# Kernel tuning notes

Measured on AMD Instinct MI355X. Metric: run time of the kernel, lower is better.

## Reference

```python
import jax, jax.numpy as jnp
import numpy as np

NUM_HEADS = 4
NUM_GROUPS = 8
EPS = 1e-5


def group_norm(x, gamma, beta):
    # x: [b, c, h, w], GroupNorm with NUM_GROUPS groups, eps=1e-5
    b, c, h, w = x.shape
    xg = x.reshape(b, NUM_GROUPS, (c // NUM_GROUPS) * h * w)
    mean = jnp.mean(xg, axis=-1, keepdims=True)
    var = jnp.var(xg, axis=-1, keepdims=True)
    xn = ((xg - mean) * jax.lax.rsqrt(var + EPS)).reshape(b, c, h, w)
    return xn * gamma[None, :, None, None] + beta[None, :, None, None]


def setup_inputs() -> dict:
    key = jax.random.key(0)
    ks = jax.random.split(key, 4)
    b, c, h, w = 4, 256, 64, 64
    x = jax.random.normal(ks[0], (b, c, h, w), dtype=jnp.float32)
    gamma = jnp.ones((c,), dtype=jnp.float32)
    beta = jnp.zeros((c,), dtype=jnp.float32)
    w_qkv = jax.random.normal(ks[1], (3 * c, c), dtype=jnp.float32) * (c ** -0.5)
    b_qkv = jnp.zeros((3 * c,), dtype=jnp.float32)
    w_proj = jax.random.normal(ks[2], (c, c), dtype=jnp.float32) * (c ** -0.5)
    b_proj = jnp.zeros((c,), dtype=jnp.float32)
    return {"x": x, "gamma": gamma, "beta": beta, "w_qkv": w_qkv,
            "b_qkv": b_qkv, "w_proj": w_proj, "b_proj": b_proj}


def reference(x, gamma, beta, w_qkv, b_qkv, w_proj, b_proj):
    b, c, h, w = x.shape
    heads = NUM_HEADS
    dim = c // heads
    n = h * w
    residual = x
    xn = group_norm(x, gamma, beta)
    # 1x1 conv == per-pixel linear: [b,c,h,w] x [3c,c] -> [b,3c,h,w]
    qkv = jnp.einsum('bchw,oc->bohw', xn, w_qkv) + b_qkv[None, :, None, None]
    # channel layout: (three, heads, dim)
    qkv = qkv.reshape(b, 3, heads, dim, n)            # [b,3,H,D,N]
    qkv = jnp.transpose(qkv, (1, 0, 2, 4, 3))         # [3,b,H,N,D]
    q, k, v = qkv[0], qkv[1], qkv[2]
    scale = dim ** -0.5
    scores = jnp.einsum('bhid,bhjd->bhij', q * scale, k)  # [b,H,N,N]
    attn = jax.nn.softmax(scores, axis=-1)
    out = jnp.einsum('bhij,bhjd->bhid', attn, v)          # [b,H,N,D]
    out = jnp.transpose(out, (0, 1, 3, 2)).reshape(b, c, h, w)
    out = jnp.einsum('bchw,oc->bohw', out, w_proj) + b_proj[None, :, None, None]
    return out + residual
```

## Files before the change

kernel.cpp:

```cpp
#include <hip/hip_runtime.h>
#include <stdint.h>

typedef unsigned short ushort_t;
typedef __attribute__((ext_vector_type(8))) short bf16x8;
typedef __attribute__((ext_vector_type(4))) float f32x4;

__device__ __forceinline__ ushort_t f2bf(float f) {
  union { float f; unsigned u; } v; v.f = f;
  unsigned r = v.u + 0x7fffu + ((v.u >> 16) & 1u);
  return (ushort_t)(r >> 16);
}
__device__ __forceinline__ unsigned bfbits(float f) {
  union { float f; unsigned u; } v; v.f = f; return v.u;
}
__device__ __forceinline__ unsigned pack_trunc(float lo, float hi) {
#if __has_builtin(__builtin_amdgcn_perm)
  return __builtin_amdgcn_perm(bfbits(hi), bfbits(lo), 0x07060302u);
#else
  return (bfbits(lo) >> 16) | (bfbits(hi) & 0xffff0000u);
#endif
}
__device__ __forceinline__ unsigned pack_rn(float lo, float hi) {
  return (unsigned)f2bf(lo) | ((unsigned)f2bf(hi) << 16);
}

#define SCALE_Q 0.18033688011112042f
#define EXP_BIAS 23.083109273961734f

__global__ __launch_bounds__(256)
void gn_stats1(const float* __restrict__ x, float2* __restrict__ partial) {
  int blk = blockIdx.x, tid = threadIdx.x;
  const float* base = x + (size_t)blk * 16384;
  float s = 0.f, ss = 0.f;
  for (int i = tid * 4; i < 16384; i += 1024) {
    float4 v = *(const float4*)(base + i);
    s  += v.x + v.y + v.z + v.w;
    ss += v.x*v.x + v.y*v.y + v.z*v.z + v.w*v.w;
  }
  __shared__ float rs[256], rss[256];
  rs[tid] = s; rss[tid] = ss;
  __syncthreads();
  for (int off = 128; off > 0; off >>= 1) {
    if (tid < off) { rs[tid] += rs[tid+off]; rss[tid] += rss[tid+off]; }
    __syncthreads();
  }
  if (tid == 0) partial[blk] = make_float2(rs[0], rss[0]);
}

__global__ __launch_bounds__(64)
void gn_stats2(const float2* __restrict__ partial, float* __restrict__ stats) {
  int g = threadIdx.x;
  if (g < 32) {
    float s = 0.f, ss = 0.f;
    #pragma unroll
    for (int k = 0; k < 8; k++) { float2 p = partial[g*8 + k]; s += p.x; ss += p.y; }
    float mean = s * (1.f/131072.f);
    float var  = ss * (1.f/131072.f) - mean*mean;
    stats[g*2]   = mean;
    stats[g*2+1] = rsqrtf(var + 1e-5f);
  }
}

__global__ __launch_bounds__(256)
void gn_apply_t(const float* __restrict__ x, const float* __restrict__ stats,
                const float* __restrict__ gamma, const float* __restrict__ beta,
                ushort_t* __restrict__ xn_t, int b0) {
  int blk = blockIdx.x;
  int tid = threadIdx.x;
  int ct = blk & 7;
  int nt = (blk >> 3) & 15;
  int bl = blk >> 7;
  int b  = b0 + bl;
  int c0 = ct * 32;
  float mean = stats[(b*8 + ct)*2];
  float rstd = stats[(b*8 + ct)*2 + 1];
  __shared__ ushort_t Ls[32][264];
  for (int idx = tid; idx < 32*64; idx += 256) {
    int cc = idx >> 6, seg = idx & 63;
    float ga = gamma[c0+cc], be = beta[c0+cc];
    float a = rstd * ga;
    float bb = be - mean * a;
    float4 v = *(const float4*)(x + ((size_t)(b*256 + c0 + cc))*4096 + nt*256 + seg*4);
    ushort4 t4 = make_ushort4(f2bf(v.x*a+bb), f2bf(v.y*a+bb), f2bf(v.z*a+bb), f2bf(v.w*a+bb));
    *(ushort4*)&Ls[cc][seg*4] = t4;
  }
  __syncthreads();
  for (int idx = tid; idx < 256*4; idx += 256) {
    int n = idx >> 2, seg = idx & 3;
    union { ushort_t u[8]; uint4 v; } pk;
    #pragma unroll
    for (int e = 0; e < 8; e++) pk.u[e] = Ls[seg*8 + e][n];
    *(uint4*)(xn_t + ((size_t)(bl*4096 + nt*256 + n))*256 + c0 + seg*8) = pk.v;
  }
}

__global__ __launch_bounds__(256)
void wconv2(const float* __restrict__ wq, const float* __restrict__ wp,
            ushort_t* __restrict__ oq, ushort_t* __restrict__ op) {
  int blk = blockIdx.x;
  const float* w; ushort_t* o; int i;
  if (blk < 192) { w = wq; o = oq; i = blk*256 + threadIdx.x; }
  else           { w = wp; o = op; i = (blk-192)*256 + threadIdx.x; }
  float4 v = *(const float4*)(w + (size_t)i*4);
  *(ushort4*)(o + (size_t)i*4) = make_ushort4(f2bf(v.x), f2bf(v.y), f2bf(v.z), f2bf(v.w));
}

__global__ __launch_bounds__(256)
void gemm_qkv(const ushort_t* __restrict__ A, const ushort_t* __restrict__ Bt,
              const float* __restrict__ bias, ushort_t* __restrict__ q,
              ushort_t* __restrict__ kbuf, ushort_t* __restrict__ vt, int b0) {
  int blk = blockIdx.x;
  int nt = blk % 12, mt = blk / 12;
  int m0 = mt*128, n0 = nt*64;
  int tid = threadIdx.x;
  int wave = tid >> 6, lane = tid & 63, quad = lane >> 4, l16 = lane & 15;
  __shared__ ushort_t As[128][40];
  __shared__ ushort_t Bs[64][40];
  __shared__ ushort_t Lt[64][136];
  f32x4 acc[2][4];
  #pragma unroll
  for (int i = 0; i < 2; i++)
    #pragma unroll
    for (int j = 0; j < 4; j++) acc[i][j] = (f32x4){0.f,0.f,0.f,0.f};

  for (int k0 = 0; k0 < 256; k0 += 32) {
    #pragma unroll
    for (int i = tid; i < 512; i += 256) {
      int row = i >> 2, seg = i & 3;
      *(uint4*)&As[row][seg*8] = *(const uint4*)(A + (size_t)(m0+row)*256 + k0 + seg*8);
    }
    {
      int row = tid >> 2, seg = tid & 3;
      *(uint4*)&Bs[row][seg*8] = *(const uint4*)(Bt + (size_t)(n0+row)*256 + k0 + seg*8);
    }
    __syncthreads();
    bf16x8 af[2], bfr[4];
    #pragma unroll
    for (int t = 0; t < 2; t++) af[t]  = *(const bf16x8*)&As[wave*32 + t*16 + l16][quad*8];
    #pragma unroll
    for (int t = 0; t < 4; t++) bfr[t] = *(const bf16x8*)&Bs[t*16 + l16][quad*8];
    #pragma unroll
    for (int ti = 0; ti < 2; ti++)
      #pragma unroll
      for (int jn = 0; jn < 4; jn++)
        acc[ti][jn] = __builtin_amdgcn_mfma_f32_16x16x32_bf16(af[ti], bfr[jn], acc[ti][jn], 0, 0, 0);
    __syncthreads();
  }

  int region = nt >> 2;
  if (region == 0) {
    #pragma unroll
    for (int jn = 0; jn < 4; jn++) {
      int n = n0 + jn*16 + l16;
      float bv = bias[n];
      #pragma unroll
      for (int ti = 0; ti < 2; ti++) {
        int mrow = m0 + wave*32 + ti*16 + quad*4;
        #pragma unroll
        for (int r = 0; r < 4; r++)
          q[(size_t)(b0*4096 + mrow + r)*256 + n] = f2bf((acc[ti][jn][r] + bv) * SCALE_Q);
      }
    }
  } else if (region == 1) {
    #pragma unroll
    for (int jn = 0; jn < 4; jn++) {
      int n = n0 + jn*16 + l16;
      float bv = bias[n];
      #pragma unroll
      for (int ti = 0; ti < 2; ti++) {
        int mrow = m0 + wave*32 + ti*16 + quad*4;
        #pragma unroll
        for (int r = 0; r < 4; r++)
          kbuf[(size_t)(b0*4096 + mrow + r)*256 + (n - 256)] = f2bf(acc[ti][jn][r] + bv);
      }
    }
  } else {
    int hh = nt - 8;
    int b_loc = m0 >> 12;
    #pragma unroll
    for (int jn = 0; jn < 4; jn++) {
      int n = n0 + jn*16 + l16;
      float bv = bias[n];
      int drow = jn*16 + l16;
      #pragma unroll
      for (int ti = 0; ti < 2; ti++) {
        int tcol = wave*32 + ti*16 + quad*4;
        uint2 w;
        w.x = pack_rn(acc[ti][jn][0] + bv, acc[ti][jn][1] + bv);
        w.y = pack_rn(acc[ti][jn][2] + bv, acc[ti][jn][3] + bv);
        *(uint2*)&Lt[drow][tcol] = w;
      }
    }
    __syncthreads();
    size_t vb_ = ((size_t)((b0 + b_loc)*4 + hh)*64)*4096 + (size_t)(m0 & 4095);
    for (int idx = tid; idx < 1024; idx += 256) {
      int dd = idx >> 4, toff = (idx & 15)*8;
      *(uint4*)(vt + vb_ + (size_t)dd*4096 + toff) = *(const uint4*)&Lt[dd][toff];
    }
  }
}

__global__ __launch_bounds__(256, 2)
void attn(ushort_t* __restrict__ q, const ushort_t* __restrict__ k,
          const ushort_t* __restrict__ vt) {
  int blk = blockIdx.x;
  int it = blk & 31;
  int h  = (blk >> 5) & 3;
  int b  = blk >> 7;
  int i0 = it * 128;
  int tid = threadIdx.x;
  int wave = tid >> 6, lane = tid & 63, quad = lane >> 4, l16 = lane & 15;

  __shared__ ushort_t Ks[2][128][68];
  __shared__ ushort_t Vs[2][64][132];
  __shared__ ushort_t Ps[4][16][72];

  ushort_t* qbase = q + (size_t)(b*4096 + i0)*256 + h*64;
  const ushort_t* kbase = k + (size_t)(b*4096)*256 + h*64;
  const ushort_t* vbase = vt + (size_t)(b*4 + h)*64*4096;

  bf16x8 qa[2][2];
  #pragma unroll
  for (int t = 0; t < 2; t++)
    #pragma unroll
    for (int kk = 0; kk < 2; kk++) {
      uint4 u = *(const uint4*)(qbase + (size_t)(wave*32 + t*16 + l16)*256 + kk*32 + quad*8);
      qa[t][kk] = *(const bf16x8*)&u;
    }

  bf16x8 ones;
  #pragma unroll
  for (int e = 0; e < 8; e++) ones[e] = (short)0x3F80;

  f32x4 o_acc[2][4];
  f32x4 l_acc[2];
  #pragma unroll
  for (int t = 0; t < 2; t++) {
    l_acc[t] = (f32x4){0.f,0.f,0.f,0.f};
    #pragma unroll
    for (int d = 0; d < 4; d++) o_acc[t][d] = (f32x4){0.f,0.f,0.f,0.f};
  }

  int sj = tid >> 3, sseg = (tid & 7)*8;
  uint4 rk[4], rv[4];
  #define LOADK(JT) { int j0n = (JT)*128; \
    rk[0] = *(const uint4*)(kbase + (size_t)(j0n + sj      )*256 + sseg); \
    rk[1] = *(const uint4*)(kbase + (size_t)(j0n + sj + 32 )*256 + sseg); \
    rk[2] = *(const uint4*)(kbase + (size_t)(j0n + sj + 64 )*256 + sseg); \
    rk[3] = *(const uint4*)(kbase + (size_t)(j0n + sj + 96 )*256 + sseg); }
  #define LOADV(JT) { int j0n = (JT)*128; \
    rv[0] = *(const uint4*)(vbase + (size_t)(sj     )*4096 + j0n + sseg); \
    rv[1] = *(const uint4*)(vbase + (size_t)(sj     )*4096 + j0n + 64 + sseg); \
    rv[2] = *(const uint4*)(vbase + (size_t)(sj + 32)*4096 + j0n + sseg); \
    rv[3] = *(const uint4*)(vbase + (size_t)(sj + 32)*4096 + j0n + 64 + sseg); }
  #define WRITEK(BI) { \
    *(uint4*)&Ks[BI][sj      ][sseg] = rk[0]; \
    *(uint4*)&Ks[BI][sj + 32 ][sseg] = rk[1]; \
    *(uint4*)&Ks[BI][sj + 64 ][sseg] = rk[2]; \
    *(uint4*)&Ks[BI][sj + 96 ][sseg] = rk[3]; }
  #define WRITEV(BI) { \
    *(uint4*)&Vs[BI][sj     ][sseg] = rv[0]; \
    *(uint4*)&Vs[BI][sj     ][64 + sseg] = rv[1]; \
    *(uint4*)&Vs[BI][sj + 32][sseg] = rv[2]; \
    *(uint4*)&Vs[BI][sj + 32][64 + sseg] = rv[3]; }

  #define COMPUTE_SUB(BI, jb) { \
    bf16x8 kb[4][2], vb[4][2]; \
    _Pragma("unroll") \
    for (int jn = 0; jn < 4; jn++) \
      _Pragma("unroll") \
      for (int kk = 0; kk < 2; kk++) { \
        kb[jn][kk] = *(const bf16x8*)&Ks[BI][(jb) + jn*16 + l16][kk*32 + quad*8]; \
        vb[jn][kk] = *(const bf16x8*)&Vs[BI][jn*16 + l16][(jb) + kk*32 + quad*8]; \
      } \
    _Pragma("unroll") \
    for (int t = 0; t < 2; t++) { \
      f32x4 s[4]; \
      _Pragma("unroll") \
      for (int jn = 0; jn < 4; jn++) { \
        f32x4 a4 = (f32x4){-EXP_BIAS, -EXP_BIAS, -EXP_BIAS, -EXP_BIAS}; \
        _Pragma("unroll") \
        for (int kk = 0; kk < 2; kk++) \
          a4 = __builtin_amdgcn_mfma_f32_16x16x32_bf16(kb[jn][kk], qa[t][kk], a4, 0, 0, 0); \
        s[jn] = a4; \
      } \
      _Pragma("unroll") \
      for (int jn = 0; jn < 4; jn++) { \
        float p0 = __builtin_exp2f(s[jn][0]); \
        float p1 = __builtin_exp2f(s[jn][1]); \
        float p2 = __builtin_exp2f(s[jn][2]); \
        float p3 = __builtin_exp2f(s[jn][3]); \
        uint2 w; \
        w.x = pack_trunc(p0, p1); \
        w.y = pack_trunc(p2, p3); \
        *(uint2*)&Ps[wave][l16][jn*16 + quad*4] = w; \
      } \
      bf16x8 pa[2]; \
      _Pragma("unroll") \
      for (int kk = 0; kk < 2; kk++) \
        pa[kk] = *(const bf16x8*)&Ps[wave][l16][kk*32 + quad*8]; \
      _Pragma("unroll") \
      for (int dn = 0; dn < 4; dn++) \
        _Pragma("unroll") \
        for (int kk = 0; kk < 2; kk++) \
          o_acc[t][dn] = __builtin_amdgcn_mfma_f32_16x16x32_bf16(vb[dn][kk], pa[kk], o_acc[t][dn], 0, 0, 0); \
      _Pragma("unroll") \
      for (int kk = 0; kk < 2; kk++) \
        l_acc[t] = __builtin_amdgcn_mfma_f32_16x16x32_bf16(ones, pa[kk], l_acc[t], 0, 0, 0); \
    } }

  LOADK(0); LOADV(0); WRITEK(0); WRITEV(0);
  __syncthreads();

  for (int jt = 0; jt < 32; jt++) {
    int cur = jt & 1;
    if (jt < 31) LOADK(jt + 1);
    COMPUTE_SUB(cur, 0);
    if (jt < 31) { WRITEK(cur ^ 1); LOADV(jt + 1); }
    COMPUTE_SUB(cur, 64);
    if (jt < 31) WRITEV(cur ^ 1);
    __syncthreads();
  }
  #undef LOADK
  #undef LOADV
  #undef WRITEK
  #undef WRITEV
  #undef COMPUTE_SUB

  #pragma unroll
  for (int t = 0; t < 2; t++) {
    float inv = 1.f / l_acc[t][0];
    size_t row = (size_t)(b*4096 + i0 + wave*32 + t*16 + l16)*256 + h*64;
    #pragma unroll
    for (int dn = 0; dn < 4; dn++) {
      ushort4 u;
      u.x = f2bf(o_acc[t][dn][0]*inv); u.y = f2bf(o_acc[t][dn][1]*inv);
      u.z = f2bf(o_acc[t][dn][2]*inv); u.w = f2bf(o_acc[t][dn][3]*inv);
      *(ushort4*)(q + row + dn*16 + quad*4) = u;
    }
  }
}

__global__ __launch_bounds__(256)
void gemm_proj(const ushort_t* __restrict__ A,
               const ushort_t* __restrict__ Bt,
               const float* __restrict__ bias, const float* __restrict__ resid,
               float* __restrict__ out, int col_base) {
  int blk = blockIdx.x;
  int mt = blk & 1, nt = blk >> 1;
  int m0 = mt*128, n0 = nt*64;
  int tid = threadIdx.x;
  int wave = tid >> 6, lane = tid & 63, quad = lane >> 4, l16 = lane & 15;
  __shared__ ushort_t As[128][40];
  __shared__ ushort_t Bs[64][40];
  f32x4 acc[2][4];
  #pragma unroll
  for (int i = 0; i < 2; i++)
    #pragma unroll
    for (int j = 0; j < 4; j++) acc[i][j] = (f32x4){0.f,0.f,0.f,0.f};

  for (int k0 = 0; k0 < 256; k0 += 32) {
    #pragma unroll
    for (int i = tid; i < 512; i += 256) {
      int row = i >> 2, seg = i & 3;
      *(uint4*)&As[row][seg*8] = *(const uint4*)(A + (size_t)(m0+row)*256 + k0 + seg*8);
    }
    {
      int row = tid >> 2, seg = tid & 3;
      *(uint4*)&Bs[row][seg*8] = *(const uint4*)(Bt + (size_t)(n0+row)*256 + k0 + seg*8);
    }
    __syncthreads();
    bf16x8 af[2], bfr[4];
    #pragma unroll
    for (int t = 0; t < 2; t++) af[t]  = *(const bf16x8*)&As[wave*32 + t*16 + l16][quad*8];
    #pragma unroll
    for (int t = 0; t < 4; t++) bfr[t] = *(const bf16x8*)&Bs[t*16 + l16][quad*8];
    #pragma unroll
    for (int ti = 0; ti < 2; ti++)
      #pragma unroll
      for (int jn = 0; jn < 4; jn++)
        acc[ti][jn] = __builtin_amdgcn_mfma_f32_16x16x32_bf16(af[ti], bfr[jn], acc[ti][jn], 0, 0, 0);
    __syncthreads();
  }
  #pragma unroll
  for (int jn = 0; jn < 4; jn++) {
    int col = col_base + n0 + jn*16 + l16;
    int bb = col >> 12;
    int np = col & 4095;
    #pragma unroll
    for (int ti = 0; ti < 2; ti++) {
      int o = m0 + wave*32 + ti*16 + quad*4;
      #pragma unroll
      for (int r = 0; r < 4; r++) {
        int oo = o + r;
        size_t addr = ((size_t)(bb*256 + oo))*4096 + np;
        out[addr] = acc[ti][jn][r] + bias[oo] + resid[addr];
      }
    }
  }
}

extern "C" void kernel_launch(void* const* d_in, const int* in_sizes, int n_in,
                              void* d_out, int out_size, void* d_ws, size_t ws_size,
                              hipStream_t stream) {
  const float* x      = (const float*)d_in[0];
  const float* gamma  = (const float*)d_in[1];
  const float* beta   = (const float*)d_in[2];
  const float* w_qkv  = (const float*)d_in[3];
  const float* b_qkv  = (const float*)d_in[4];
  const float* w_proj = (const float*)d_in[5];
  const float* b_proj = (const float*)d_in[6];
  float* out = (float*)d_out;

  char* ws = (char*)d_ws;
  float*  stats    = (float*)ws;
  float2* partial  = (float2*)(ws + 1024);
  ushort_t* wqkv_bf  = (ushort_t*)(ws + 4096);
  ushort_t* wproj_bf = (ushort_t*)(ws + 397312);
  char* big = ws + 528384;

  gn_stats1<<<dim3(256), dim3(256), 0, stream>>>(x, partial);
  gn_stats2<<<dim3(1), dim3(64), 0, stream>>>(partial, stats);
  wconv2<<<dim3(256), dim3(256), 0, stream>>>(w_qkv, w_proj, wqkv_bf, wproj_bf);

  if (ws_size >= (size_t)528384 + 3*(size_t)8388608 + (size_t)4194304) {
    ushort_t* q    = (ushort_t*)big;
    ushort_t* kbuf = (ushort_t*)(big + (size_t)8388608);
    ushort_t* vt   = (ushort_t*)(big + (size_t)16777216);
    ushort_t* xn   = (ushort_t*)(big + (size_t)25165824);
    for (int c = 0; c < 2; c++) {
      int b0 = c * 2;
      gn_apply_t<<<dim3(256), dim3(256), 0, stream>>>(x, stats, gamma, beta, xn, b0);
      gemm_qkv<<<dim3(768), dim3(256), 0, stream>>>(xn, wqkv_bf, b_qkv, q, kbuf, vt, b0);
    }
    attn<<<dim3(512), dim3(256), 0, stream>>>(q, kbuf, vt);
    gemm_proj<<<dim3(512), dim3(256), 0, stream>>>(wproj_bf, q, b_proj, x, out, 0);
  } else {
    ushort_t* q_c  = (ushort_t*)big;
    ushort_t* k_c  = (ushort_t*)(big + (size_t)2097152);
    ushort_t* vt_c = (ushort_t*)(big + (size_t)4194304);
    ushort_t* xn_c = (ushort_t*)(big + (size_t)6291456);
    for (int b0 = 0; b0 < 4; b0++) {
      gn_apply_t<<<dim3(128), dim3(256), 0, stream>>>(x, stats, gamma, beta, xn_c, b0);
      gemm_qkv<<<dim3(384), dim3(256), 0, stream>>>(xn_c, wqkv_bf, b_qkv, q_c, k_c, vt_c, 0);
      attn<<<dim3(128), dim3(256), 0, stream>>>(q_c, k_c, vt_c);
      gemm_proj<<<dim3(128), dim3(256), 0, stream>>>(wproj_bf, q_c, b_proj, x, out, b0*4096);
    }
  }
}
```

Before: 256.4 us.

## Rewrite attention inner loop with 32x32x16 MFMA and register-resident P

```diff
diff --git a/kernel.cpp b/kernel.cpp
--- a/kernel.cpp
+++ b/kernel.cpp
@@ -4,6 +4,7 @@
 typedef unsigned short ushort_t;
 typedef __attribute__((ext_vector_type(8))) short bf16x8;
 typedef __attribute__((ext_vector_type(4))) float f32x4;
+typedef __attribute__((ext_vector_type(16))) float f32x16;
 
 __device__ __forceinline__ ushort_t f2bf(float f) {
   union { float f; unsigned u; } v; v.f = f;
@@ -22,6 +23,14 @@
 }
 __device__ __forceinline__ unsigned pack_rn(float lo, float hi) {
   return (unsigned)f2bf(lo) | ((unsigned)f2bf(hi) << 16);
+}
+__device__ __forceinline__ void swap32(unsigned &a, unsigned &b) {
+#if __has_builtin(__builtin_amdgcn_permlane32_swap)
+  auto r = __builtin_amdgcn_permlane32_swap(a, b, false, false);
+  a = r[0]; b = r[1];
+#else
+  asm volatile("v_permlane32_swap_b32 %0, %1" : "+v"(a), "+v"(b));
+#endif
 }
 
 #define SCALE_Q 0.18033688011112042f
@@ -209,105 +218,94 @@
   int b  = blk >> 7;
   int i0 = it * 128;
   int tid = threadIdx.x;
-  int wave = tid >> 6, lane = tid & 63, quad = lane >> 4, l16 = lane & 15;
-
-  __shared__ ushort_t Ks[2][128][68];
-  __shared__ ushort_t Vs[2][64][132];
-  __shared__ ushort_t Ps[4][16][72];
-
-  ushort_t* qbase = q + (size_t)(b*4096 + i0)*256 + h*64;
+  int wave = tid >> 6, lane = tid & 63;
+  int q32 = lane & 31, hi = lane >> 5;
+
+  __shared__ ushort_t Ks[2][128][72];
+  __shared__ ushort_t Vs[2][64][144];
+
   const ushort_t* kbase = k + (size_t)(b*4096)*256 + h*64;
   const ushort_t* vbase = vt + (size_t)(b*4 + h)*64*4096;
-
-  bf16x8 qa[2][2];
-  #pragma unroll
-  for (int t = 0; t < 2; t++)
-    #pragma unroll
-    for (int kk = 0; kk < 2; kk++) {
-      uint4 u = *(const uint4*)(qbase + (size_t)(wave*32 + t*16 + l16)*256 + kk*32 + quad*8);
-      qa[t][kk] = *(const bf16x8*)&u;
-    }
-
-  bf16x8 ones;
-  #pragma unroll
-  for (int e = 0; e < 8; e++) ones[e] = (short)0x3F80;
-
-  f32x4 o_acc[2][4];
-  f32x4 l_acc[2];
-  #pragma unroll
-  for (int t = 0; t < 2; t++) {
-    l_acc[t] = (f32x4){0.f,0.f,0.f,0.f};
-    #pragma unroll
-    for (int d = 0; d < 4; d++) o_acc[t][d] = (f32x4){0.f,0.f,0.f,0.f};
-  }
-
-  int sj = tid >> 3, sseg = (tid & 7)*8;
+  ushort_t* qrow = q + (size_t)(b*4096 + i0 + wave*32 + q32)*256 + h*64;
+
+  bf16x8 qb[4];
+  #pragma unroll
+  for (int s = 0; s < 4; s++) {
+    uint4 u = *(const uint4*)(qrow + s*16 + hi*8);
+    qb[s] = *(const bf16x8*)&u;
+  }
+
+  f32x16 o_acc[2];
+  #pragma unroll
+  for (int d = 0; d < 2; d++)
+    #pragma unroll
+    for (int r = 0; r < 16; r++) o_acc[d][r] = 0.f;
+  float lsum = 0.f;
+
+  int sr = tid >> 3, sc = (tid & 7) * 8;
+  int vr = tid >> 4, vc = (tid & 15) * 8;
   uint4 rk[4], rv[4];
   #define LOADK(JT) { int j0n = (JT)*128; \
-    rk[0] = *(const uint4*)(kbase + (size_t)(j0n + sj      )*256 + sseg); \
-    rk[1] = *(const uint4*)(kbase + (size_t)(j0n + sj + 32 )*256 + sseg); \
-    rk[2] = *(const uint4*)(kbase + (size_t)(j0n + sj + 64 )*256 + sseg); \
-    rk[3] = *(const uint4*)(kbase + (size_t)(j0n + sj + 96 )*256 + sseg); }
+    rk[0] = *(const uint4*)(kbase + (size_t)(j0n + sr      )*256 + sc); \
+    rk[1] = *(const uint4*)(kbase + (size_t)(j0n + sr + 32 )*256 + sc); \
+    rk[2] = *(const uint4*)(kbase + (size_t)(j0n + sr + 64 )*256 + sc); \
+    rk[3] = *(const uint4*)(kbase + (size_t)(j0n + sr + 96 )*256 + sc); }
+  #define WRITEK(BI) { \
+    *(uint4*)&Ks[BI][sr      ][sc] = rk[0]; \
+    *(uint4*)&Ks[BI][sr + 32 ][sc] = rk[1]; \
+    *(uint4*)&Ks[BI][sr + 64 ][sc] = rk[2]; \
+    *(uint4*)&Ks[BI][sr + 96 ][sc] = rk[3]; }
   #define LOADV(JT) { int j0n = (JT)*128; \
-    rv[0] = *(const uint4*)(vbase + (size_t)(sj     )*4096 + j0n + sseg); \
-    rv[1] = *(const uint4*)(vbase + (size_t)(sj     )*4096 + j0n + 64 + sseg); \
-    rv[2] = *(const uint4*)(vbase + (size_t)(sj + 32)*4096 + j0n + sseg); \
-    rv[3] = *(const uint4*)(vbase + (size_t)(sj + 32)*4096 + j0n + 64 + sseg); }
-  #define WRITEK(BI) { \
-    *(uint4*)&Ks[BI][sj      ][sseg] = rk[0]; \
-    *(uint4*)&Ks[BI][sj + 32 ][sseg] = rk[1]; \
-    *(uint4*)&Ks[BI][sj + 64 ][sseg] = rk[2]; \
-    *(uint4*)&Ks[BI][sj + 96 ][sseg] = rk[3]; }
+    rv[0] = *(const uint4*)(vbase + (size_t)(vr     )*4096 + j0n + vc); \
+    rv[1] = *(const uint4*)(vbase + (size_t)(vr + 16)*4096 + j0n + vc); \
+    rv[2] = *(const uint4*)(vbase + (size_t)(vr + 32)*4096 + j0n + vc); \
+    rv[3] = *(const uint4*)(vbase + (size_t)(vr + 48)*4096 + j0n + vc); }
   #define WRITEV(BI) { \
-    *(uint4*)&Vs[BI][sj     ][sseg] = rv[0]; \
-    *(uint4*)&Vs[BI][sj     ][64 + sseg] = rv[1]; \
-    *(uint4*)&Vs[BI][sj + 32][sseg] = rv[2]; \
-    *(uint4*)&Vs[BI][sj + 32][64 + sseg] = rv[3]; }
-
-  #define COMPUTE_SUB(BI, jb) { \
-    bf16x8 kb[4][2], vb[4][2]; \
+    *(uint4*)&Vs[BI][vr     ][vc] = rv[0]; \
+    *(uint4*)&Vs[BI][vr + 16][vc] = rv[1]; \
+    *(uint4*)&Vs[BI][vr + 32][vc] = rv[2]; \
+    *(uint4*)&Vs[BI][vr + 48][vc] = rv[3]; }
+
+  #define COMPUTE_SUB32(BI, JB) { \
+    bf16x8 kb0 = *(const bf16x8*)&Ks[BI][(JB) + q32][hi*8]; \
+    bf16x8 kb1 = *(const bf16x8*)&Ks[BI][(JB) + q32][16 + hi*8]; \
+    bf16x8 kb2 = *(const bf16x8*)&Ks[BI][(JB) + q32][32 + hi*8]; \
+    bf16x8 kb3 = *(const bf16x8*)&Ks[BI][(JB) + q32][48 + hi*8]; \
+    f32x16 s_; \
     _Pragma("unroll") \
-    for (int jn = 0; jn < 4; jn++) \
-      _Pragma("unroll") \
-      for (int kk = 0; kk < 2; kk++) { \
-        kb[jn][kk] = *(const bf16x8*)&Ks[BI][(jb) + jn*16 + l16][kk*32 + quad*8]; \
-        vb[jn][kk] = *(const bf16x8*)&Vs[BI][jn*16 + l16][(jb) + kk*32 + quad*8]; \
-      } \
+    for (int r = 0; r < 16; r++) s_[r] = -EXP_BIAS; \
+    s_ = __builtin_amdgcn_mfma_f32_32x32x16_bf16(kb0, qb[0], s_, 0, 0, 0); \
+    s_ = __builtin_amdgcn_mfma_f32_32x32x16_bf16(kb1, qb[1], s_, 0, 0, 0); \
+    s_ = __builtin_amdgcn_mfma_f32_32x32x16_bf16(kb2, qb[2], s_, 0, 0, 0); \
+    s_ = __builtin_amdgcn_mfma_f32_32x32x16_bf16(kb3, qb[3], s_, 0, 0, 0); \
+    float pt[16]; \
     _Pragma("unroll") \
-    for (int t = 0; t < 2; t++) { \
-      f32x4 s[4]; \
-      _Pragma("unroll") \
-      for (int jn = 0; jn < 4; jn++) { \
-        f32x4 a4 = (f32x4){-EXP_BIAS, -EXP_BIAS, -EXP_BIAS, -EXP_BIAS}; \
-        _Pragma("unroll") \
-        for (int kk = 0; kk < 2; kk++) \
-          a4 = __builtin_amdgcn_mfma_f32_16x16x32_bf16(kb[jn][kk], qa[t][kk], a4, 0, 0, 0); \
-        s[jn] = a4; \
-      } \
-      _Pragma("unroll") \
-      for (int jn = 0; jn < 4; jn++) { \
-        float p0 = __builtin_exp2f(s[jn][0]); \
-        float p1 = __builtin_exp2f(s[jn][1]); \
-        float p2 = __builtin_exp2f(s[jn][2]); \
-        float p3 = __builtin_exp2f(s[jn][3]); \
-        uint2 w; \
-        w.x = pack_trunc(p0, p1); \
-        w.y = pack_trunc(p2, p3); \
-        *(uint2*)&Ps[wave][l16][jn*16 + quad*4] = w; \
-      } \
-      bf16x8 pa[2]; \
-      _Pragma("unroll") \
-      for (int kk = 0; kk < 2; kk++) \
-        pa[kk] = *(const bf16x8*)&Ps[wave][l16][kk*32 + quad*8]; \
-      _Pragma("unroll") \
-      for (int dn = 0; dn < 4; dn++) \
-        _Pragma("unroll") \
-        for (int kk = 0; kk < 2; kk++) \
-          o_acc[t][dn] = __builtin_amdgcn_mfma_f32_16x16x32_bf16(vb[dn][kk], pa[kk], o_acc[t][dn], 0, 0, 0); \
-      _Pragma("unroll") \
-      for (int kk = 0; kk < 2; kk++) \
-        l_acc[t] = __builtin_amdgcn_mfma_f32_16x16x32_bf16(ones, pa[kk], l_acc[t], 0, 0, 0); \
-    } }
+    for (int r = 0; r < 16; r++) { \
+      float pe = __builtin_exp2f(s_[r]); \
+      s_[r] = pe; \
+      union { unsigned u; float f; } tv; tv.u = bfbits(pe) & 0xffff0000u; \
+      pt[r] = tv.f; \
+    } \
+    lsum += ((((pt[0]+pt[1])+(pt[2]+pt[3])) + ((pt[4]+pt[5])+(pt[6]+pt[7]))) \
+          + (((pt[8]+pt[9])+(pt[10]+pt[11])) + ((pt[12]+pt[13])+(pt[14]+pt[15])))); \
+    unsigned pkA = pack_trunc(s_[0],  s_[1]),  pkB = pack_trunc(s_[2],  s_[3]); \
+    unsigned pkC = pack_trunc(s_[4],  s_[5]),  pkD = pack_trunc(s_[6],  s_[7]); \
+    unsigned pkE = pack_trunc(s_[8],  s_[9]),  pkF = pack_trunc(s_[10], s_[11]); \
+    unsigned pkG = pack_trunc(s_[12], s_[13]), pkH = pack_trunc(s_[14], s_[15]); \
+    swap32(pkA, pkC); swap32(pkB, pkD);    \
+    swap32(pkE, pkG); swap32(pkF, pkH);    \
+    union { unsigned u[4]; bf16x8 v; } pb0_, pb1_; \
+    pb0_.u[0] = pkA; pb0_.u[1] = pkB; pb0_.u[2] = pkC; pb0_.u[3] = pkD; \
+    pb1_.u[0] = pkE; pb1_.u[1] = pkF; pb1_.u[2] = pkG; pb1_.u[3] = pkH; \
+    bf16x8 vb00 = *(const bf16x8*)&Vs[BI][q32     ][(JB) + hi*8]; \
+    bf16x8 vb01 = *(const bf16x8*)&Vs[BI][q32     ][(JB) + 16 + hi*8]; \
+    bf16x8 vb10 = *(const bf16x8*)&Vs[BI][32 + q32][(JB) + hi*8]; \
+    bf16x8 vb11 = *(const bf16x8*)&Vs[BI][32 + q32][(JB) + 16 + hi*8]; \
+    o_acc[0] = __builtin_amdgcn_mfma_f32_32x32x16_bf16(vb00, pb0_.v, o_acc[0], 0, 0, 0); \
+    o_acc[0] = __builtin_amdgcn_mfma_f32_32x32x16_bf16(vb01, pb1_.v, o_acc[0], 0, 0, 0); \
+    o_acc[1] = __builtin_amdgcn_mfma_f32_32x32x16_bf16(vb10, pb0_.v, o_acc[1], 0, 0, 0); \
+    o_acc[1] = __builtin_amdgcn_mfma_f32_32x32x16_bf16(vb11, pb1_.v, o_acc[1], 0, 0, 0); \
+  }
 
   LOADK(0); LOADV(0); WRITEK(0); WRITEV(0);
   __syncthreads();
@@ -315,9 +313,11 @@
   for (int jt = 0; jt < 32; jt++) {
     int cur = jt & 1;
     if (jt < 31) LOADK(jt + 1);
-    COMPUTE_SUB(cur, 0);
+    COMPUTE_SUB32(cur, 0)
+    COMPUTE_SUB32(cur, 32)
     if (jt < 31) { WRITEK(cur ^ 1); LOADV(jt + 1); }
-    COMPUTE_SUB(cur, 64);
+    COMPUTE_SUB32(cur, 64)
+    COMPUTE_SUB32(cur, 96)
     if (jt < 31) WRITEV(cur ^ 1);
     __syncthreads();
   }
@@ -325,20 +325,22 @@
   #undef LOADV
   #undef WRITEK
   #undef WRITEV
-  #undef COMPUTE_SUB
-
-  #pragma unroll
-  for (int t = 0; t < 2; t++) {
-    float inv = 1.f / l_acc[t][0];
-    size_t row = (size_t)(b*4096 + i0 + wave*32 + t*16 + l16)*256 + h*64;
-    #pragma unroll
-    for (int dn = 0; dn < 4; dn++) {
+  #undef COMPUTE_SUB32
+
+  unsigned ua = __float_as_uint(lsum), ub = ua;
+  swap32(ua, ub);
+  float ltot = __uint_as_float(ua) + __uint_as_float(ub);
+  float inv = 1.f / ltot;
+
+  #pragma unroll
+  for (int dblk = 0; dblk < 2; dblk++)
+    #pragma unroll
+    for (int g = 0; g < 4; g++) {
       ushort4 u;
-      u.x = f2bf(o_acc[t][dn][0]*inv); u.y = f2bf(o_acc[t][dn][1]*inv);
-      u.z = f2bf(o_acc[t][dn][2]*inv); u.w = f2bf(o_acc[t][dn][3]*inv);
-      *(ushort4*)(q + row + dn*16 + quad*4) = u;
-    }
-  }
+      u.x = f2bf(o_acc[dblk][g*4+0]*inv); u.y = f2bf(o_acc[dblk][g*4+1]*inv);
+      u.z = f2bf(o_acc[dblk][g*4+2]*inv); u.w = f2bf(o_acc[dblk][g*4+3]*inv);
+      *(ushort4*)(qrow + dblk*32 + g*8 + hi*4) = u;
+    }
 }
 
 __global__ __launch_bounds__(256)
```

New measurement: 306.5 us. 19.5% more time.
